# Optimization experiments

Measured on AMD Instinct MI355X. Metric: run time of the kernel, lower is better.

Reference implementation:

```python
import jax, jax.numpy as jnp
import numpy as np

L = 2          # num layers
HID = 96       # hidden channels per layer


def _gate_conv(x, w, bias):
    # x: [B, Cin, H, W], w: [4*HID, Cin, 3, 3] -> [B, 4*HID, H, W], SAME padding
    y = jax.lax.conv_general_dilated(
        x, w, window_strides=(1, 1), padding='SAME',
        dimension_numbers=('NCHW', 'OIHW', 'NCHW'))
    return y + bias[None, :, None, None]


def setup_inputs() -> dict:
    key = jax.random.key(0)
    k_inp, k_w = jax.random.split(key)
    B, T, C, H, Wd = 8, 12, 96, 48, 48
    inp = jax.random.normal(k_inp, (B, T, C, H, Wd), dtype=jnp.float32)
    h0 = jnp.zeros((L, B, HID, H, Wd), dtype=jnp.float32)
    c0 = jnp.zeros((L, B, HID, H, Wd), dtype=jnp.float32)
    # gate conv weights: per layer [4*HID, C + HID, 3, 3] (fan-in scaled)
    W = jax.random.normal(k_w, (L, 4 * HID, C + HID, 3, 3), dtype=jnp.float32)
    W = W * (1.0 / np.sqrt((C + HID) * 9)).astype(np.float32)
    b = jnp.zeros((L, 4 * HID), dtype=jnp.float32)
    return {'inp': inp, 'h0': h0, 'c0': c0, 'W': W, 'b': b}


def reference(inp, h0, c0, W, b):
    # inp: [B,T,C,H,W]; h0,c0: [L,B,HID,H,W]; W: [L,4H,C+H,3,3]; b: [L,4H]
    xs = jnp.moveaxis(inp, 1, 0)  # [T,B,C,H,W]

    def step(carry, x_t):
        h, c = carry  # each [L,B,HID,H,W]
        layer_in = x_t
        new_h, new_c = [], []
        for l in range(L):
            z = jnp.concatenate([layer_in, h[l]], axis=1)  # [B, C+HID, H, W]
            gates = _gate_conv(z, W[l], b[l])              # [B, 4*HID, H, W]
            i, f, o, g = jnp.split(gates, 4, axis=1)
            c_n = jax.nn.sigmoid(f) * c[l] + jax.nn.sigmoid(i) * jnp.tanh(g)
            h_n = jax.nn.sigmoid(o) * jnp.tanh(c_n)
            new_h.append(h_n)
            new_c.append(c_n)
            layer_in = h_n
        h = jnp.stack(new_h)
        c = jnp.stack(new_c)
        return (h, c), h

    (h_f, c_f), hs = jax.lax.scan(step, (h0, c0), xs)
    # hs: [T,L,B,HID,H,W] -> all hidden states per layer, batch_first
    all_hidden = jnp.moveaxis(jnp.moveaxis(hs, 1, 0), 2, 1)  # [L,B,T,HID,H,W]
    return all_hidden, h_f, c_f
```

## Files before the change

### kernel.cpp

```cpp
#include <hip/hip_runtime.h>
#include <hip/hip_bf16.h>
#include <stdint.h>

#define HWDIM 48
#define PLANE 2304
#define NB 8
#define NT 12
#define CHID 96
#define OC 384
#define KTOT 1728
#define BN 144
#define NBLK_JOB 128
#define NCHUNK 54
#define PPLANE 2500
#define PGRP 3
#define IMG_E ((size_t)PGRP * PPLANE * 32)
#define SLOT_E ((size_t)NB * IMG_E)
#define BT ((size_t)CHID * PLANE)

typedef __attribute__((ext_vector_type(8))) short short8;
typedef __attribute__((ext_vector_type(4))) float f32x4;
typedef __attribute__((ext_vector_type(4))) unsigned int u32x4;

__device__ __forceinline__ unsigned short f2bf(float f) {
  union { float f; uint32_t u; } x; x.f = f;
  uint32_t u = x.u;
  return (unsigned short)((u + 0x7FFFu + ((u >> 16) & 1u)) >> 16);
}

__global__ void convlstm_wconv(const float* __restrict__ W, unsigned short* __restrict__ Wb, int total) {
  int idx = blockIdx.x * 256 + threadIdx.x;
  if (idx >= total) return;
  const int PER_L = NCHUNK * 24 * 64 * 8;
  int layer = idx / PER_L;
  int r = idx - layer * PER_L;
  int jj = r & 7;
  int l = (r >> 3) & 63;
  int fr = r >> 9;
  int rm = fr % 24;
  int c = fr / 24;
  int oc = rm * 16 + (l & 15);
  int oco = (oc & 3) * 96 + (oc >> 2);
  int k = c * 32 + ((l >> 4) << 3) + jj;
  int tap = k / 192;
  int ic = k - tap * 192;
  float v = W[(((size_t)layer * OC + oco) * 192 + ic) * 9 + tap];
  Wb[idx] = f2bf(v);
}

__global__ void pack_interior(const float* __restrict__ src, unsigned short* __restrict__ dst,
                              int mode, int t_base, int slot_mask) {
  __shared__ float T[32][65];
  int bid = blockIdx.x;
  int tile = bid % 36;
  int grp  = (bid / 36) % 3;
  int imgi = bid / 108;
  int slot; size_t srcoff;
  if (mode == 0) {
    int b = imgi & 7; int t = t_base + (imgi >> 3);
    srcoff = ((size_t)b * NT + t) * BT;
    slot = (t & slot_mask) * NB + b;
  } else {
    int b = imgi & 7; int l = imgi >> 3;
    srcoff = (size_t)imgi * BT;
    slot = (l * 2 + 1) * NB + b;
  }
  const float* s = src + srcoff + (size_t)grp * 32 * PLANE + tile * 64;
  const int tid = threadIdx.x;
#pragma unroll
  for (int r = 0; r < 8; ++r) {
    int ch = r * 4 + (tid >> 6);
    T[ch][tid & 63] = s[(size_t)ch * PLANE + (tid & 63)];
  }
  __syncthreads();
  int p = tid >> 2, sq = tid & 3;
  int pos = tile * 64 + p;
  int py = pos / 48 + 1, px = pos % 48 + 1;
  unsigned short v[8];
#pragma unroll
  for (int i = 0; i < 8; ++i) v[i] = f2bf(T[sq * 8 + i][p]);
  *(short8*)(dst + ((size_t)slot * PGRP + grp) * (PPLANE * 32) + (py * 50 + px) * 32 + sq * 8) = *(short8*)v;
}

__global__ void border_zero(unsigned short* dst, int nplanes) {
  int idx = blockIdx.x * 256 + threadIdx.x;
  if (idx >= nplanes * 784) return;
  int plane = idx / 784;
  int r = idx - plane * 784;
  int g = r >> 2, sq = r & 3;
  int py, px;
  if (g < 50)       { py = 0;       px = g; }
  else if (g < 100) { py = 49;      px = g - 50; }
  else if (g < 148) { py = g - 99;  px = 0; }
  else              { py = g - 147; px = 49; }
  u32x4 z = {0, 0, 0, 0};
  *(u32x4*)(dst + (size_t)plane * (PPLANE * 32) + (py * 50 + px) * 32 + sq * 8) = z;
}

struct Job {
  const unsigned short* xp;
  const unsigned short* hp;
  unsigned short* hw;
  const short8* w;
  const float* bias;
  float* c_base;
  float* h_out; long long ho_bs;
  float* hf;
};

__global__ __launch_bounds__(512, 1) void convlstm_step(Job j0, Job j1) {
  __shared__ __align__(16) char smem[96000];
  unsigned short* HALO = (unsigned short*)smem;
  unsigned short* HP = (unsigned short*)smem;

  const int tid = threadIdx.x;
  const Job j = (blockIdx.x < NBLK_JOB) ? j0 : j1;
  const int n0 = (blockIdx.x % NBLK_JOB) * BN;
  const int lane = tid & 63;
  const int wid = tid >> 6;

  const int bb = n0 / PLANE;
  const int spb = n0 - bb * PLANE;
  const int y0 = spb / 48;

  const unsigned short* xb = j.xp + (size_t)bb * IMG_E;
  const unsigned short* hb = j.hp + (size_t)bb * IMG_E;
  for (int it = 0; it < 3; ++it) {
    int pg = tid + it * 512;
    if (pg < 1500) {
      int tensor = pg / 750;
      int rem = pg - tensor * 750;
      int grp = rem / 250;
      int r2 = rem - grp * 250;
      int rr = r2 / 50;
      int px = r2 - rr * 50;
      int gs = tensor * 3 + grp;
      const unsigned short* src = (tensor ? hb : xb) + (size_t)grp * (PPLANE * 32)
                                  + (size_t)((y0 + rr) * 50 + px) * 32;
#pragma unroll
      for (int q = 0; q < 4; ++q) {
        short8 v = *(const short8*)(src + q * 8);
        *(short8*)&HALO[(size_t)(((gs * 4 + q) * 5 + rr) * 50 + px) * 8] = v;
      }
    }
  }

  f32x4 acc[3][9];
#pragma unroll
  for (int rm = 0; rm < 3; ++rm) {
    const int ch = wid * 12 + rm * 4 + (lane >> 4);
    f32x4 bi;
#pragma unroll
    for (int r = 0; r < 4; ++r) bi[r] = j.bias[r * 96 + ch];
#pragma unroll
    for (int cn = 0; cn < 9; ++cn) acc[rm][cn] = bi;
  }

  const short8* aw = j.w + (size_t)(wid * 3) * 64 + lane;
  short8 a_cur[3];
#pragma unroll
  for (int rm = 0; rm < 3; ++rm) a_cur[rm] = aw[rm * 64];

  __syncthreads();

  const int lofs = (lane >> 4) * 2000 + (lane & 15) * 8;

  auto bload = [&](int c, short8* bf) {
    const int tap = c / 6, gs2 = c - tap * 6;
    const int kh = tap / 3, kw = tap - kh * 3;
#pragma unroll
    for (int cn = 0; cn < 9; ++cn) {
      const int off = gs2 * 8000 + ((cn / 3) + kh) * 400 + ((cn % 3) * 16 + kw) * 8 + lofs;
      bf[cn] = *(const short8*)&HALO[off];
    }
  };

  short8 b_cur[9];
  bload(0, b_cur);

#pragma unroll 1
  for (int c = 0; c < NCHUNK; ++c) {
    const int c1 = (c + 1 < NCHUNK) ? (c + 1) : (NCHUNK - 1);
    short8 a_nxt[3];
#pragma unroll
    for (int rm = 0; rm < 3; ++rm) a_nxt[rm] = aw[(size_t)c1 * 1536 + rm * 64];
    short8 b_nxt[9];
    bload(c1, b_nxt);

    __builtin_amdgcn_s_setprio(1);
#pragma unroll
    for (int cn = 0; cn < 9; ++cn)
#pragma unroll
      for (int rm = 0; rm < 3; ++rm)
        acc[rm][cn] = __builtin_amdgcn_mfma_f32_16x16x32_bf16(a_cur[rm], b_cur[cn], acc[rm][cn], 0, 0, 0);
    __builtin_amdgcn_s_setprio(0);

#pragma unroll
    for (int rm = 0; rm < 3; ++rm) a_cur[rm] = a_nxt[rm];
#pragma unroll
    for (int cn = 0; cn < 9; ++cn) b_cur[cn] = b_nxt[cn];
  }

  __syncthreads();

#pragma unroll
  for (int rm = 0; rm < 3; ++rm) {
    const int ch = wid * 12 + rm * 4 + (lane >> 4);
    float* cb_ = j.c_base + (size_t)bb * (CHID * PLANE) + (size_t)ch * PLANE;
    float* hb_ = j.h_out + (size_t)bb * j.ho_bs + (size_t)ch * PLANE;
    float* hf_ = j.hf ? (j.hf + (size_t)bb * (CHID * PLANE) + (size_t)ch * PLANE) : nullptr;
#pragma unroll
    for (int cn = 0; cn < 9; ++cn) {
      const int col = cn * 16 + (lane & 15);
      const int spe = spb + col;
      const float gi = acc[rm][cn][0];
      const float gf = acc[rm][cn][1];
      const float go = acc[rm][cn][2];
      const float gg = acc[rm][cn][3];
      const float si = 1.f / (1.f + __expf(-gi));
      const float sf = 1.f / (1.f + __expf(-gf));
      const float so = 1.f / (1.f + __expf(-go));
      const float e2g = __expf(2.f * gg);
      const float tg = 1.f - 2.f / (e2g + 1.f);
      const float cold = cb_[spe];
      const float cn2 = sf * cold + si * tg;
      const float e2c = __expf(2.f * cn2);
      const float tc = 1.f - 2.f / (e2c + 1.f);
      const float hn = so * tc;
      cb_[spe] = cn2;
      hb_[spe] = hn;
      if (hf_) hf_[spe] = hn;
      HP[col * 96 + ch] = f2bf(hn);
    }
  }
  __syncthreads();

#pragma unroll
  for (int it = 0; it < 4; ++it) {
    int gi = tid + it * 512;
    if (gi < 1728) {
      int gq = gi / 144;
      int p  = gi - gq * 144;
      int grp = gq >> 2, sq = gq & 3;
      int pos = spb + p;
      int py = pos / 48 + 1, px = pos % 48 + 1;
      short8 v = *(short8*)&HP[p * 96 + grp * 32 + sq * 8];
      *(short8*)(j.hw + (size_t)bb * IMG_E + (size_t)grp * (PPLANE * 32) + (py * 50 + px) * 32 + sq * 8) = v;
    }
  }
}

extern "C" void kernel_launch(void* const* d_in, const int* in_sizes, int n_in,
                              void* d_out, int out_size, void* d_ws, size_t ws_size,
                              hipStream_t stream) {
  const float* inp  = (const float*)d_in[0];
  const float* h0   = (const float*)d_in[1];
  const float* c0   = (const float*)d_in[2];
  const float* W    = (const float*)d_in[3];
  const float* bias = (const float*)d_in[4];

  float* AH = (float*)d_out;
  float* HF = AH + (size_t)2 * NB * NT * BT;
  float* CF = HF + (size_t)2 * NB * BT;

  const size_t WB_BYTES = (size_t)2 * NCHUNK * 24 * 64 * 8 * 2;
  const size_t PH_BYTES = (size_t)4 * SLOT_E * 2;
  const size_t PX_BIG   = (size_t)NT * SLOT_E * 2;
  const bool big = ws_size >= WB_BYTES + PH_BYTES + PX_BIG;
  unsigned short* Wb = (unsigned short*)d_ws;
  unsigned short* ph = (unsigned short*)((char*)d_ws + WB_BYTES);
  unsigned short* px = (unsigned short*)((char*)d_ws + WB_BYTES + PH_BYTES);

  {
    int total = 2 * NCHUNK * 24 * 64 * 8;
    convlstm_wconv<<<(total + 255) / 256, 256, 0, stream>>>(W, Wb, total);
  }
  {
    int np_ph = 4 * NB * 3;
    border_zero<<<(np_ph * 784 + 255) / 256, 256, 0, stream>>>(ph, np_ph);
    int np_px = (big ? NT : 2) * NB * 3;
    border_zero<<<(np_px * 784 + 255) / 256, 256, 0, stream>>>(px, np_px);
  }
  {
    int n_img = big ? (NT * NB) : (2 * NB);
    pack_interior<<<n_img * 108, 256, 0, stream>>>(inp, px, 0, 0, big ? 15 : 1);
    pack_interior<<<2 * NB * 108, 256, 0, stream>>>(h0, ph, 1, 0, 0);
  }
  hipMemcpyAsync(CF, c0, (size_t)2 * NB * BT * sizeof(float), hipMemcpyDeviceToDevice, stream);

  const size_t PER_L = (size_t)NCHUNK * 24 * 64;

  auto mkjob = [&](int l, int t) -> Job {
    Job j;
    if (l == 0) j.xp = px + (size_t)(big ? t : (t & 1)) * SLOT_E;
    else        j.xp = ph + (size_t)(0 * 2 + (t & 1)) * SLOT_E;
    j.hp = ph + (size_t)(l * 2 + ((t + 1) & 1)) * SLOT_E;
    j.hw = ph + (size_t)(l * 2 + (t & 1)) * SLOT_E;
    j.w = (const short8*)Wb + (size_t)l * PER_L;
    j.bias = bias + l * OC;
    j.c_base = CF + (size_t)l * NB * BT;
    j.h_out = AH + (size_t)l * NB * NT * BT + (size_t)t * BT;
    j.ho_bs = (long long)NT * BT;
    j.hf = (t == NT - 1) ? (HF + (size_t)l * NB * BT) : nullptr;
    return j;
  };

  for (int k = 0; k <= NT; ++k) {
    const bool hasA = (k <= NT - 1);
    const bool hasB = (k >= 1);
    Job ja, jb;
    int njobs = 0;
    if (hasA) { ja = mkjob(0, k); njobs = 1; }
    if (hasB) {
      Job xj = mkjob(1, k - 1);
      if (njobs) jb = xj; else ja = xj;
      njobs++;
    }
    if (njobs == 1) jb = ja;
    convlstm_step<<<njobs * NBLK_JOB, 512, 0, stream>>>(ja, jb);
    if (!big && k + 2 <= NT - 1)
      pack_interior<<<NB * 108, 256, 0, stream>>>(inp, px, 0, k + 2, 1);
  }
}
```

Before: 679.9 us.

## Overlap per-group halo staging with MFMA compute and prefetch old cell state

```diff
diff --git a/kernel.cpp b/kernel.cpp
--- a/kernel.cpp
+++ b/kernel.cpp
@@ -125,25 +125,23 @@
 
   const unsigned short* xb = j.xp + (size_t)bb * IMG_E;
   const unsigned short* hb = j.hp + (size_t)bb * IMG_E;
-  for (int it = 0; it < 3; ++it) {
-    int pg = tid + it * 512;
-    if (pg < 1500) {
-      int tensor = pg / 750;
-      int rem = pg - tensor * 750;
-      int grp = rem / 250;
-      int r2 = rem - grp * 250;
-      int rr = r2 / 50;
-      int px = r2 - rr * 50;
-      int gs = tensor * 3 + grp;
-      const unsigned short* src = (tensor ? hb : xb) + (size_t)grp * (PPLANE * 32)
-                                  + (size_t)((y0 + rr) * 50 + px) * 32;
-#pragma unroll
-      for (int q = 0; q < 4; ++q) {
-        short8 v = *(const short8*)(src + q * 8);
-        *(short8*)&HALO[(size_t)(((gs * 4 + q) * 5 + rr) * 50 + px) * 8] = v;
+
+  auto stage = [&](int gs) {
+#pragma unroll
+    for (int it = 0; it < 2; ++it) {
+      int gi = tid + it * 512;
+      if (gi < 1000) {
+        int q = gi & 3;
+        int g16 = gi >> 2;
+        int rr = g16 / 50;
+        int px = g16 - rr * 50;
+        const unsigned short* base = (gs < 3) ? (xb + (size_t)gs * (PPLANE * 32))
+                                              : (hb + (size_t)(gs - 3) * (PPLANE * 32));
+        short8 v = *(const short8*)(base + (size_t)((y0 + rr) * 50 + px) * 32 + q * 8);
+        *(short8*)&HALO[(size_t)((((gs * 4 + q) * 5 + rr) * 50 + px)) * 8] = v;
       }
     }
-  }
+  };
 
   f32x4 acc[3][9];
 #pragma unroll
@@ -159,48 +157,66 @@
   const short8* aw = j.w + (size_t)(wid * 3) * 64 + lane;
   short8 a_cur[3];
 #pragma unroll
-  for (int rm = 0; rm < 3; ++rm) a_cur[rm] = aw[rm * 64];
-
+  for (int rm = 0; rm < 3; ++rm) a_cur[rm] = aw[(size_t)(0 * 6 + 0) * 1536 + rm * 64];
+
+  const int lofs = (lane >> 4) * 2000 + (lane & 15) * 8;
+
+  auto bload = [&](int gs, int tap, short8* bf) {
+    const int kh = tap / 3, kw = tap - kh * 3;
+#pragma unroll
+    for (int cn = 0; cn < 9; ++cn) {
+      const int off = gs * 8000 + ((cn / 3) + kh) * 400 + ((cn % 3) * 16 + kw) * 8 + lofs;
+      bf[cn] = *(const short8*)&HALO[off];
+    }
+  };
+
+  stage(0);
   __syncthreads();
 
-  const int lofs = (lane >> 4) * 2000 + (lane & 15) * 8;
-
-  auto bload = [&](int c, short8* bf) {
-    const int tap = c / 6, gs2 = c - tap * 6;
-    const int kh = tap / 3, kw = tap - kh * 3;
-#pragma unroll
-    for (int cn = 0; cn < 9; ++cn) {
-      const int off = gs2 * 8000 + ((cn / 3) + kh) * 400 + ((cn % 3) * 16 + kw) * 8 + lofs;
-      bf[cn] = *(const short8*)&HALO[off];
-    }
-  };
-
-  short8 b_cur[9];
-  bload(0, b_cur);
-
 #pragma unroll 1
-  for (int c = 0; c < NCHUNK; ++c) {
-    const int c1 = (c + 1 < NCHUNK) ? (c + 1) : (NCHUNK - 1);
-    short8 a_nxt[3];
-#pragma unroll
-    for (int rm = 0; rm < 3; ++rm) a_nxt[rm] = aw[(size_t)c1 * 1536 + rm * 64];
-    short8 b_nxt[9];
-    bload(c1, b_nxt);
-
-    __builtin_amdgcn_s_setprio(1);
-#pragma unroll
-    for (int cn = 0; cn < 9; ++cn)
+  for (int gs = 0; gs < 6; ++gs) {
+    if (gs < 5) stage(gs + 1);
+
+    short8 b_cur[9];
+    bload(gs, 0, b_cur);
+
+#pragma unroll 1
+    for (int tap = 0; tap < 9; ++tap) {
+      int nt_tap = (tap < 8) ? tap + 1 : 0;
+      int nt_gs  = (tap < 8) ? gs : (gs < 5 ? gs + 1 : gs);
+      short8 a_nxt[3];
 #pragma unroll
       for (int rm = 0; rm < 3; ++rm)
-        acc[rm][cn] = __builtin_amdgcn_mfma_f32_16x16x32_bf16(a_cur[rm], b_cur[cn], acc[rm][cn], 0, 0, 0);
-    __builtin_amdgcn_s_setprio(0);
-
-#pragma unroll
-    for (int rm = 0; rm < 3; ++rm) a_cur[rm] = a_nxt[rm];
-#pragma unroll
-    for (int cn = 0; cn < 9; ++cn) b_cur[cn] = b_nxt[cn];
-  }
-
+        a_nxt[rm] = aw[(size_t)(nt_tap * 6 + nt_gs) * 1536 + rm * 64];
+      short8 b_nxt[9];
+      if (tap < 8) bload(gs, tap + 1, b_nxt);
+
+      __builtin_amdgcn_s_setprio(1);
+#pragma unroll
+      for (int cn = 0; cn < 9; ++cn)
+#pragma unroll
+        for (int rm = 0; rm < 3; ++rm)
+          acc[rm][cn] = __builtin_amdgcn_mfma_f32_16x16x32_bf16(a_cur[rm], b_cur[cn], acc[rm][cn], 0, 0, 0);
+      __builtin_amdgcn_s_setprio(0);
+
+#pragma unroll
+      for (int rm = 0; rm < 3; ++rm) a_cur[rm] = a_nxt[rm];
+      if (tap < 8) {
+#pragma unroll
+        for (int cn = 0; cn < 9; ++cn) b_cur[cn] = b_nxt[cn];
+      }
+    }
+    __syncthreads();
+  }
+
+  float cold[3][9];
+#pragma unroll
+  for (int rm = 0; rm < 3; ++rm) {
+    const int ch = wid * 12 + rm * 4 + (lane >> 4);
+    const float* cb_ = j.c_base + (size_t)bb * (CHID * PLANE) + (size_t)ch * PLANE + spb + (lane & 15);
+#pragma unroll
+    for (int cn = 0; cn < 9; ++cn) cold[rm][cn] = cb_[cn * 16];
+  }
   __syncthreads();
 
 #pragma unroll
@@ -222,8 +238,7 @@
       const float so = 1.f / (1.f + __expf(-go));
       const float e2g = __expf(2.f * gg);
       const float tg = 1.f - 2.f / (e2g + 1.f);
-      const float cold = cb_[spe];
-      const float cn2 = sf * cold + si * tg;
+      const float cn2 = sf * cold[rm][cn] + si * tg;
       const float e2c = __expf(2.f * cn2);
       const float tc = 1.f - 2.f / (e2c + 1.f);
       const float hn = so * tc;
```

Result: slower. 695.7 us (+2.3%).

## Replace per-timestep launches with a persistent cooperative kernel using grid sync

Applied to the files above, without the earlier changes.

```diff
diff --git a/kernel.cpp b/kernel.cpp
--- a/kernel.cpp
+++ b/kernel.cpp
@@ -1,6 +1,9 @@
 #include <hip/hip_runtime.h>
 #include <hip/hip_bf16.h>
+#include <hip/hip_cooperative_groups.h>
 #include <stdint.h>
+
+namespace cg = cooperative_groups;
 
 #define HWDIM 48
 #define PLANE 2304
@@ -17,6 +20,7 @@
 #define IMG_E ((size_t)PGRP * PPLANE * 32)
 #define SLOT_E ((size_t)NB * IMG_E)
 #define BT ((size_t)CHID * PLANE)
+#define PER_L ((size_t)NCHUNK * 24 * 64)
 
 typedef __attribute__((ext_vector_type(8))) short short8;
 typedef __attribute__((ext_vector_type(4))) float f32x4;
@@ -31,9 +35,9 @@
 __global__ void convlstm_wconv(const float* __restrict__ W, unsigned short* __restrict__ Wb, int total) {
   int idx = blockIdx.x * 256 + threadIdx.x;
   if (idx >= total) return;
-  const int PER_L = NCHUNK * 24 * 64 * 8;
-  int layer = idx / PER_L;
-  int r = idx - layer * PER_L;
+  const int PER_LI = NCHUNK * 24 * 64 * 8;
+  int layer = idx / PER_LI;
+  int r = idx - layer * PER_LI;
   int jj = r & 7;
   int l = (r >> 3) & 63;
   int fr = r >> 9;
@@ -97,6 +101,182 @@
   *(u32x4*)(dst + (size_t)plane * (PPLANE * 32) + (py * 50 + px) * 32 + sq * 8) = z;
 }
 
+struct PArgs {
+  const unsigned short* px;
+  unsigned short* ph;
+  const short8* wb;
+  const float* bias;
+  const float* c0;
+  float* AH;
+  float* HF;
+  float* CF;
+};
+
+__global__ __launch_bounds__(512, 1) void convlstm_persist(PArgs pa) {
+  cg::grid_group grid = cg::this_grid();
+  __shared__ __align__(16) char smem[96000];
+  unsigned short* HALO = (unsigned short*)smem;
+  unsigned short* HP = (unsigned short*)smem;
+
+  const int tid = threadIdx.x;
+  const int bid = blockIdx.x;
+  const int layer = (bid >= NBLK_JOB) ? 1 : 0;
+  const int tile = bid - layer * NBLK_JOB;
+  const int n0 = tile * BN;
+  const int lane = tid & 63;
+  const int wid = tid >> 6;
+
+  const int bb = n0 / PLANE;
+  const int spb = n0 - bb * PLANE;
+  const int y0 = spb / 48;
+
+  const short8* aw = pa.wb + (size_t)layer * PER_L + (size_t)(wid * 3) * 64 + lane;
+  const float* bias = pa.bias + layer * OC;
+  const int lofs = (lane >> 4) * 2000 + (lane & 15) * 8;
+
+  float creg[3][9];
+#pragma unroll
+  for (int rm = 0; rm < 3; ++rm) {
+    const int ch = wid * 12 + rm * 4 + (lane >> 4);
+    const float* cs = pa.c0 + (size_t)layer * NB * BT + (size_t)bb * (CHID * PLANE)
+                    + (size_t)ch * PLANE + spb + (lane & 15);
+#pragma unroll
+    for (int cn = 0; cn < 9; ++cn) creg[rm][cn] = cs[cn * 16];
+  }
+
+#pragma unroll 1
+  for (int k = 0; k <= NT; ++k) {
+    const int t = layer ? (k - 1) : k;
+    const bool active = layer ? (k >= 1) : (k <= NT - 1);
+    if (active) {
+      const unsigned short* xp = layer ? (pa.ph + (size_t)(t & 1) * SLOT_E)
+                                       : (pa.px + (size_t)t * SLOT_E);
+      const unsigned short* hp = pa.ph + (size_t)(layer * 2 + ((t + 1) & 1)) * SLOT_E;
+      unsigned short* hw = pa.ph + (size_t)(layer * 2 + (t & 1)) * SLOT_E;
+      float* h_out = pa.AH + (size_t)layer * NB * NT * BT + (size_t)t * BT;
+      const bool last = (t == NT - 1);
+
+      const unsigned short* xb = xp + (size_t)bb * IMG_E;
+      const unsigned short* hb = hp + (size_t)bb * IMG_E;
+      for (int it = 0; it < 3; ++it) {
+        int pg = tid + it * 512;
+        if (pg < 1500) {
+          int tensor = pg / 750;
+          int rem = pg - tensor * 750;
+          int grp = rem / 250;
+          int r2 = rem - grp * 250;
+          int rr = r2 / 50;
+          int px2 = r2 - rr * 50;
+          int gs = tensor * 3 + grp;
+          const unsigned short* src = (tensor ? hb : xb) + (size_t)grp * (PPLANE * 32)
+                                      + (size_t)((y0 + rr) * 50 + px2) * 32;
+#pragma unroll
+          for (int q = 0; q < 4; ++q) {
+            short8 v = *(const short8*)(src + q * 8);
+            *(short8*)&HALO[(size_t)(((gs * 4 + q) * 5 + rr) * 50 + px2) * 8] = v;
+          }
+        }
+      }
+
+      f32x4 acc[3][9];
+#pragma unroll
+      for (int rm = 0; rm < 3; ++rm) {
+        const int ch = wid * 12 + rm * 4 + (lane >> 4);
+        f32x4 bi;
+#pragma unroll
+        for (int r = 0; r < 4; ++r) bi[r] = bias[r * 96 + ch];
+#pragma unroll
+        for (int cn = 0; cn < 9; ++cn) acc[rm][cn] = bi;
+      }
+      short8 a_cur[3];
+#pragma unroll
+      for (int rm = 0; rm < 3; ++rm) a_cur[rm] = aw[rm * 64];
+
+      __syncthreads();
+
+#pragma unroll 1
+      for (int c = 0; c < NCHUNK; ++c) {
+        const int c1 = (c + 1 < NCHUNK) ? (c + 1) : c;
+        short8 a_nxt[3];
+#pragma unroll
+        for (int rm = 0; rm < 3; ++rm) a_nxt[rm] = aw[(size_t)c1 * 1536 + rm * 64];
+
+        const int tap = c / 6, gs2 = c - tap * 6;
+        const int kh = tap / 3, kw = tap - kh * 3;
+        short8 bf[9];
+#pragma unroll
+        for (int cn = 0; cn < 9; ++cn) {
+          const int off = gs2 * 8000 + ((cn / 3) + kh) * 400 + ((cn % 3) * 16 + kw) * 8 + lofs;
+          bf[cn] = *(const short8*)&HALO[off];
+        }
+
+        __builtin_amdgcn_s_setprio(1);
+#pragma unroll
+        for (int cn = 0; cn < 9; ++cn)
+#pragma unroll
+          for (int rm = 0; rm < 3; ++rm)
+            acc[rm][cn] = __builtin_amdgcn_mfma_f32_16x16x32_bf16(a_cur[rm], bf[cn], acc[rm][cn], 0, 0, 0);
+        __builtin_amdgcn_s_setprio(0);
+
+#pragma unroll
+        for (int rm = 0; rm < 3; ++rm) a_cur[rm] = a_nxt[rm];
+      }
+
+      __syncthreads();
+
+#pragma unroll
+      for (int rm = 0; rm < 3; ++rm) {
+        const int ch = wid * 12 + rm * 4 + (lane >> 4);
+        float* hb_ = h_out + (size_t)bb * (NT * BT) + (size_t)ch * PLANE;
+        float* hf_ = last ? (pa.HF + (size_t)layer * NB * BT + (size_t)bb * (CHID * PLANE) + (size_t)ch * PLANE) : nullptr;
+        float* cf_ = last ? (pa.CF + (size_t)layer * NB * BT + (size_t)bb * (CHID * PLANE) + (size_t)ch * PLANE) : nullptr;
+#pragma unroll
+        for (int cn = 0; cn < 9; ++cn) {
+          const int col = cn * 16 + (lane & 15);
+          const int spe = spb + col;
+          const float gi = acc[rm][cn][0];
+          const float gf = acc[rm][cn][1];
+          const float go = acc[rm][cn][2];
+          const float gg = acc[rm][cn][3];
+          const float si = 1.f / (1.f + __expf(-gi));
+          const float sf = 1.f / (1.f + __expf(-gf));
+          const float so = 1.f / (1.f + __expf(-go));
+          const float e2g = __expf(2.f * gg);
+          const float tg = 1.f - 2.f / (e2g + 1.f);
+          const float cn2 = sf * creg[rm][cn] + si * tg;
+          creg[rm][cn] = cn2;
+          const float e2c = __expf(2.f * cn2);
+          const float tc = 1.f - 2.f / (e2c + 1.f);
+          const float hn = so * tc;
+          hb_[spe] = hn;
+          if (hf_) hf_[spe] = hn;
+          if (cf_) cf_[spe] = cn2;
+          HP[col * 96 + ch] = f2bf(hn);
+        }
+      }
+      __syncthreads();
+
+#pragma unroll
+      for (int it = 0; it < 4; ++it) {
+        int gi = tid + it * 512;
+        if (gi < 1728) {
+          int gq = gi / 144;
+          int p  = gi - gq * 144;
+          int grp = gq >> 2, sq = gq & 3;
+          int pos = spb + p;
+          int py = pos / 48 + 1, px2 = pos % 48 + 1;
+          short8 v = *(short8*)&HP[p * 96 + grp * 32 + sq * 8];
+          *(short8*)(hw + (size_t)bb * IMG_E + (size_t)grp * (PPLANE * 32) + (py * 50 + px2) * 32 + sq * 8) = v;
+        }
+      }
+    }
+    if (k < NT) {
+      __threadfence();
+      grid.sync();
+    }
+  }
+}
+
 struct Job {
   const unsigned short* xp;
   const unsigned short* hp;
@@ -165,42 +345,42 @@
 
   const int lofs = (lane >> 4) * 2000 + (lane & 15) * 8;
 
-  auto bload = [&](int c, short8* bf) {
+#pragma unroll 1
+  for (int c = 0; c < NCHUNK; ++c) {
+    const int c1 = (c + 1 < NCHUNK) ? (c + 1) : c;
+    short8 a_nxt[3];
+#pragma unroll
+    for (int rm = 0; rm < 3; ++rm) a_nxt[rm] = aw[(size_t)c1 * 1536 + rm * 64];
+
     const int tap = c / 6, gs2 = c - tap * 6;
     const int kh = tap / 3, kw = tap - kh * 3;
+    short8 bf[9];
 #pragma unroll
     for (int cn = 0; cn < 9; ++cn) {
       const int off = gs2 * 8000 + ((cn / 3) + kh) * 400 + ((cn % 3) * 16 + kw) * 8 + lofs;
       bf[cn] = *(const short8*)&HALO[off];
     }
-  };
-
-  short8 b_cur[9];
-  bload(0, b_cur);
-
-#pragma unroll 1
-  for (int c = 0; c < NCHUNK; ++c) {
-    const int c1 = (c + 1 < NCHUNK) ? (c + 1) : (NCHUNK - 1);
-    short8 a_nxt[3];
-#pragma unroll
-    for (int rm = 0; rm < 3; ++rm) a_nxt[rm] = aw[(size_t)c1 * 1536 + rm * 64];
-    short8 b_nxt[9];
-    bload(c1, b_nxt);
 
     __builtin_amdgcn_s_setprio(1);
 #pragma unroll
     for (int cn = 0; cn < 9; ++cn)
 #pragma unroll
       for (int rm = 0; rm < 3; ++rm)
-        acc[rm][cn] = __builtin_amdgcn_mfma_f32_16x16x32_bf16(a_cur[rm], b_cur[cn], acc[rm][cn], 0, 0, 0);
+        acc[rm][cn] = __builtin_amdgcn_mfma_f32_16x16x32_bf16(a_cur[rm], bf[cn], acc[rm][cn], 0, 0, 0);
     __builtin_amdgcn_s_setprio(0);
 
 #pragma unroll
     for (int rm = 0; rm < 3; ++rm) a_cur[rm] = a_nxt[rm];
-#pragma unroll
-    for (int cn = 0; cn < 9; ++cn) b_cur[cn] = b_nxt[cn];
-  }
-
+  }
+
+  float cold[3][9];
+#pragma unroll
+  for (int rm = 0; rm < 3; ++rm) {
+    const int ch = wid * 12 + rm * 4 + (lane >> 4);
+    const float* cb_ = j.c_base + (size_t)bb * (CHID * PLANE) + (size_t)ch * PLANE + spb + (lane & 15);
+#pragma unroll
+    for (int cn = 0; cn < 9; ++cn) cold[rm][cn] = cb_[cn * 16];
+  }
   __syncthreads();
 
 #pragma unroll
@@ -222,8 +402,7 @@
       const float so = 1.f / (1.f + __expf(-go));
       const float e2g = __expf(2.f * gg);
       const float tg = 1.f - 2.f / (e2g + 1.f);
-      const float cold = cb_[spe];
-      const float cn2 = sf * cold + si * tg;
+      const float cn2 = sf * cold[rm][cn] + si * tg;
       const float e2c = __expf(2.f * cn2);
       const float tc = 1.f - 2.f / (e2c + 1.f);
       const float hn = so * tc;
@@ -286,13 +465,22 @@
     pack_interior<<<n_img * 108, 256, 0, stream>>>(inp, px, 0, 0, big ? 15 : 1);
     pack_interior<<<2 * NB * 108, 256, 0, stream>>>(h0, ph, 1, 0, 0);
   }
+
+  if (big) {
+    PArgs pa;
+    pa.px = px; pa.ph = ph; pa.wb = (const short8*)Wb; pa.bias = bias;
+    pa.c0 = c0; pa.AH = AH; pa.HF = HF; pa.CF = CF;
+    void* kargs[] = { (void*)&pa };
+    hipLaunchCooperativeKernel((void*)convlstm_persist, dim3(2 * NBLK_JOB), dim3(512),
+                               kargs, 0, stream);
+    return;
+  }
+
   hipMemcpyAsync(CF, c0, (size_t)2 * NB * BT * sizeof(float), hipMemcpyDeviceToDevice, stream);
-
-  const size_t PER_L = (size_t)NCHUNK * 24 * 64;
 
   auto mkjob = [&](int l, int t) -> Job {
     Job j;
-    if (l == 0) j.xp = px + (size_t)(big ? t : (t & 1)) * SLOT_E;
+    if (l == 0) j.xp = px + (size_t)(t & 1) * SLOT_E;
     else        j.xp = ph + (size_t)(0 * 2 + (t & 1)) * SLOT_E;
     j.hp = ph + (size_t)(l * 2 + ((t + 1) & 1)) * SLOT_E;
     j.hw = ph + (size_t)(l * 2 + (t & 1)) * SLOT_E;
@@ -318,7 +506,7 @@
     }
     if (njobs == 1) jb = ja;
     convlstm_step<<<njobs * NBLK_JOB, 512, 0, stream>>>(ja, jb);
-    if (!big && k + 2 <= NT - 1)
+    if (k + 2 <= NT - 1)
       pack_interior<<<NB * 108, 256, 0, stream>>>(inp, px, 0, k + 2, 1);
   }
 }
```

New measurement: 1.779 ms. 2.62x slower.
